# Performance work log

Hardware: AMD Instinct MI355X
Metric: run time of the kernel (lower is better)

## Reference

```python
import jax, jax.numpy as jnp
import numpy as np

NUM_HEADS = 8
NVIEW = 5
EPS = 1e-6


def setup_inputs() -> dict:
    key = jax.random.key(0)
    k1, k2, k3 = jax.random.split(key, 3)
    BV, HW, C = 20, 4096, 256
    x = jax.random.normal(k1, (BV, HW, C), dtype=jnp.float32)
    # torch.nn.Linear default init ~ U(-1/sqrt(in), 1/sqrt(in)); scale randn similarly
    W_qkv = jax.random.normal(k2, (C, 3 * C), dtype=jnp.float32) * (1.0 / np.sqrt(C))
    W_proj = jax.random.normal(k3, (C, C), dtype=jnp.float32) * (1.0 / np.sqrt(C))
    b_proj = jnp.zeros((C,), dtype=jnp.float32)
    return {"x": x, "W_qkv": W_qkv, "W_proj": W_proj, "b_proj": b_proj}


def reference(x, W_qkv, W_proj, b_proj):
    BV, HW, C = x.shape
    V = NVIEW
    B = BV // V
    H = NUM_HEADS
    d = C // H
    L = V * HW

    # merge views into one long sequence per batch element
    xb = x.reshape(B, L, C)

    # qkv projection (qkv_bias=False) -> [B, L, 3, H, d]
    qkv = (xb @ W_qkv).reshape(B, L, 3, H, d)
    q = qkv[:, :, 0]  # [B, L, H, d]
    k = qkv[:, :, 1]
    v = qkv[:, :, 2]

    # elu + 1 feature map, computed in float32 (as in the autocast-disabled block)
    q = (jax.nn.elu(q) + 1.0).astype(jnp.float32)
    k = (jax.nn.elu(k) + 1.0).astype(jnp.float32)
    v = v.astype(jnp.float32)

    # linear attention: kv = sum_l k_l (x) v_l  -> [B, H, m, d]
    kv = jnp.einsum('nlhd,nlhm->nhmd', k, v)
    # normalizer z = 1 / (q . sum_l k_l)  -> [B, L, H]
    k_sum = k.sum(axis=1)  # [B, H, d]
    z = 1.0 / (jnp.einsum('nlhd,nhd->nlh', q, k_sum) + EPS)
    # output y -> [B, L, H, m]
    y = jnp.einsum('nlhd,nhmd,nlh->nlhm', q, kv, z)

    y = y.reshape(BV, HW, C)
    return y @ W_proj + b_proj
```

## Files before the change

kernel.cpp:

```cpp
#include <hip/hip_runtime.h>

#define M_ROWS 81920
#define KDIM 256
#define NQKV 768
#define LROWS 20480
#define EPSV 1e-6f
#define KV_CHUNKS 160

using bf16x8 = __attribute__((ext_vector_type(8))) short;
using f32x4  = __attribute__((ext_vector_type(4))) float;

static __device__ __forceinline__ unsigned short f2bf(float f) {
  union { float f; unsigned int u; } c; c.f = f;
  unsigned int u = c.u;
  u += 0x7fff + ((u >> 16) & 1);
  return (unsigned short)(u >> 16);
}
static __device__ __forceinline__ float bf2f(unsigned short h) {
  union { unsigned int u; float f; } c; c.u = ((unsigned int)h) << 16;
  return c.f;
}

static __device__ __forceinline__ void async_cp16(const void* g, void* l) {
  __builtin_amdgcn_global_load_lds(
      (const __attribute__((address_space(1))) void*)(unsigned long long)g,
      (__attribute__((address_space(3))) void*)(unsigned int)(unsigned long long)l,
      16, 0, 0);
}

__global__ void cvt_x(const float* __restrict__ x, unsigned short* __restrict__ xb) {
  long i = ((long)blockIdx.x * blockDim.x + threadIdx.x) * 4;
  float4 v = *(const float4*)(x + i);
  ushort4 o;
  o.x = f2bf(v.x); o.y = f2bf(v.y); o.z = f2bf(v.z); o.w = f2bf(v.w);
  *(ushort4*)(xb + i) = o;
}

__global__ void transpose_w(const float* __restrict__ w, unsigned short* __restrict__ wt,
                            int K, int N) {
  int k = blockIdx.x;
  for (int n = threadIdx.x; n < N; n += blockDim.x)
    wt[(size_t)n * K + k] = f2bf(w[(size_t)k * N + n]);
}

template <int EPI>
__global__ __launch_bounds__(256, 3)
void gemm_bt(const unsigned short* __restrict__ A,
             const unsigned short* __restrict__ Bt,
             void* __restrict__ C,
             const float* __restrict__ bias,
             int N) {
  __shared__ unsigned short As[128 * 32];
  __shared__ unsigned short Bs[128 * 32];
  const int K = 256;
  int t = threadIdx.x;
  int lane = t & 63;
  int w = t >> 6;
  int m0 = blockIdx.y * 128;
  int n0 = blockIdx.x * 128;
  const unsigned short* Bp = Bt;
  if (EPI == 1) Bp += (size_t)(blockIdx.y / 160) * 256 * 256;

  f32x4 acc[4][4];
#pragma unroll
  for (int i = 0; i < 4; i++)
#pragma unroll
    for (int j = 0; j < 4; j++) acc[i][j] = (f32x4){0.f, 0.f, 0.f, 0.f};

  int wm = w & 1, wn = w >> 1;
  int fm = lane & 15;
  int fk = (lane >> 4) * 8;
  int r0a = t >> 2, p0 = t & 3;
  int r1a = (t + 256) >> 2, p1 = t & 3;

  for (int kt = 0; kt < 8; kt++) {
    int k0 = kt * 32;
    __syncthreads();
    async_cp16(A + (size_t)(m0 + r0a) * K + k0 + p0 * 8, As + (size_t)t * 8);
    async_cp16(A + (size_t)(m0 + r1a) * K + k0 + p1 * 8, As + (size_t)(t + 256) * 8);
    async_cp16(Bp + (size_t)(n0 + r0a) * K + k0 + p0 * 8, Bs + (size_t)t * 8);
    async_cp16(Bp + (size_t)(n0 + r1a) * K + k0 + p1 * 8, Bs + (size_t)(t + 256) * 8);
    __syncthreads();
    bf16x8 af[4], bfr[4];
#pragma unroll
    for (int i = 0; i < 4; i++)
      af[i] = *(const bf16x8*)(As + (wm * 64 + i * 16 + fm) * 32 + fk);
#pragma unroll
    for (int j = 0; j < 4; j++)
      bfr[j] = *(const bf16x8*)(Bs + (wn * 64 + j * 16 + fm) * 32 + fk);
#pragma unroll
    for (int i = 0; i < 4; i++)
#pragma unroll
      for (int j = 0; j < 4; j++)
        acc[i][j] = __builtin_amdgcn_mfma_f32_16x16x32_bf16(af[i], bfr[j], acc[i][j], 0, 0, 0);
  }

  int quad = lane >> 4;
  int col = lane & 15;
#pragma unroll
  for (int i = 0; i < 4; i++) {
#pragma unroll
    for (int j = 0; j < 4; j++) {
      int gm_base = m0 + wm * 64 + i * 16 + quad * 4;
      int gn = n0 + wn * 64 + j * 16 + col;
#pragma unroll
      for (int r = 0; r < 4; r++) {
        float v = acc[i][j][r];
        int gm = gm_base + r;
        if (EPI == 0) {
          if (gn < 512) v = (v > 0.f) ? v + 1.f : __expf(v);
          ((unsigned short*)C)[(size_t)gm * N + gn] = f2bf(v);
        } else {
          ((float*)C)[(size_t)gm * N + gn] = v + bias[gn];
        }
      }
    }
  }
}

__global__ __launch_bounds__(512)
void kv_reduce(const unsigned short* __restrict__ qkv, float* __restrict__ kvp) {
  __shared__ unsigned short s[32 * 512];
  int chunk = blockIdx.x;
  int n = blockIdx.y;
  int t = threadIdx.x;
  int lane = t & 63;
  int w = t >> 6;
  long r0 = (long)n * LROWS + (long)chunk * 128;

  float acc[4][4] = {};
  float ks[4] = {};
  int mg = lane >> 3;
  int m0 = mg * 4, d0 = (lane & 7) * 4;

  for (int tile = 0; tile < 4; tile++) {
    __syncthreads();
#pragma unroll
    for (int q = 0; q < 4; q++) {
      int c = t + q * 512;
      int row = c >> 6, part = c & 63;
      async_cp16(qkv + (size_t)(r0 + tile * 32 + row) * 768 + 256 + part * 8,
                 s + (size_t)c * 8);
    }
    __syncthreads();
#pragma unroll 4
    for (int row = 0; row < 32; row++) {
      ushort4 kk = *(const ushort4*)(s + row * 512 + w * 32 + d0);
      ushort4 vv = *(const ushort4*)(s + row * 512 + 256 + w * 32 + m0);
      float kf[4] = {bf2f(kk.x), bf2f(kk.y), bf2f(kk.z), bf2f(kk.w)};
      float vf[4] = {bf2f(vv.x), bf2f(vv.y), bf2f(vv.z), bf2f(vv.w)};
#pragma unroll
      for (int i = 0; i < 4; i++)
#pragma unroll
        for (int j = 0; j < 4; j++) acc[i][j] += vf[i] * kf[j];
      if (mg == 0) {
        ks[0] += kf[0]; ks[1] += kf[1]; ks[2] += kf[2]; ks[3] += kf[3];
      }
    }
  }
  float* o = kvp + ((size_t)(n * KV_CHUNKS + chunk) * 8 + w) * 1056;
#pragma unroll
  for (int i = 0; i < 4; i++)
#pragma unroll
    for (int j = 0; j < 4; j++) o[(m0 + i) * 32 + d0 + j] = acc[i][j];
  if (mg == 0) {
#pragma unroll
    for (int j = 0; j < 4; j++) o[1024 + d0 + j] = ks[j];
  }
}

__global__ __launch_bounds__(256)
void kv_combine(const float* __restrict__ kvp, float* __restrict__ kv,
                float* __restrict__ ksum) {
  int pair = blockIdx.x;
  int n = pair >> 3, h = pair & 7;
  int t = threadIdx.x;
  float a0 = 0.f, a1 = 0.f, a2 = 0.f, a3 = 0.f, a4 = 0.f;
  const float* base = kvp + ((size_t)(n * KV_CHUNKS) * 8 + h) * 1056;
  for (int c = 0; c < KV_CHUNKS; c++) {
    const float* p = base + (size_t)c * 8 * 1056;
    a0 += p[t]; a1 += p[t + 256]; a2 += p[t + 512]; a3 += p[t + 768];
    if (t < 32) a4 += p[1024 + t];
  }
  float* kvo = kv + (size_t)pair * 1024;
  kvo[t] = a0; kvo[t + 256] = a1; kvo[t + 512] = a2; kvo[t + 768] = a3;
  if (t < 32) ksum[pair * 32 + t] = a4;
}

__global__ __launch_bounds__(256)
void make_g(const float* __restrict__ kv, const float* __restrict__ wproj,
            unsigned short* __restrict__ gt) {
  __shared__ float kvs[1024];
  int pair = blockIdx.x;
  int n = pair >> 3, h = pair & 7;
  int c = threadIdx.x;
  for (int i = c; i < 1024; i += 256) kvs[i] = kv[(size_t)pair * 1024 + i];
  __syncthreads();
  float acc[32];
#pragma unroll
  for (int d = 0; d < 32; d++) acc[d] = 0.f;
  for (int m = 0; m < 32; m++) {
    float wp = wproj[(size_t)(h * 32 + m) * 256 + c];
#pragma unroll
    for (int d = 0; d < 32; d++) acc[d] += kvs[m * 32 + d] * wp;
  }
  unsigned short* o = gt + ((size_t)n * 256 + c) * 256 + h * 32;
#pragma unroll
  for (int d = 0; d < 32; d++) o[d] = f2bf(acc[d]);
}

__global__ __launch_bounds__(256)
void scale_q(const unsigned short* __restrict__ qkv, const float* __restrict__ ksum,
             unsigned short* __restrict__ qp) {
  int t = threadIdx.x;
  int lane32 = t & 31;
  int rsub = t >> 5;
  long r0 = (long)blockIdx.x * 64;
  for (int p = 0; p < 8; p++) {
    long r = r0 + p * 8 + rsub;
    int n = (int)(r / LROWS);
    const unsigned short* q = qkv + r * 768 + lane32 * 8;
    ushort4 a = *(const ushort4*)(q);
    ushort4 b = *(const ushort4*)(q + 4);
    float qf[8] = {bf2f(a.x), bf2f(a.y), bf2f(a.z), bf2f(a.w),
                   bf2f(b.x), bf2f(b.y), bf2f(b.z), bf2f(b.w)};
    const float* ks = ksum + n * 256 + lane32 * 8;
    float sacc = 0.f;
#pragma unroll
    for (int i = 0; i < 8; i++) sacc += qf[i] * ks[i];
    sacc += __shfl_xor(sacc, 1);
    sacc += __shfl_xor(sacc, 2);
    float z = 1.f / (sacc + EPSV);
    ushort4 oa, ob;
    oa.x = f2bf(qf[0] * z); oa.y = f2bf(qf[1] * z);
    oa.z = f2bf(qf[2] * z); oa.w = f2bf(qf[3] * z);
    ob.x = f2bf(qf[4] * z); ob.y = f2bf(qf[5] * z);
    ob.z = f2bf(qf[6] * z); ob.w = f2bf(qf[7] * z);
    unsigned short* o = qp + r * 256 + lane32 * 8;
    *(ushort4*)o = oa;
    *(ushort4*)(o + 4) = ob;
  }
}

extern "C" void kernel_launch(void* const* d_in, const int* in_sizes, int n_in,
                              void* d_out, int out_size, void* d_ws, size_t ws_size,
                              hipStream_t stream) {
  (void)in_sizes; (void)n_in; (void)out_size; (void)ws_size;
  const float* x = (const float*)d_in[0];
  const float* Wqkv = (const float*)d_in[1];
  const float* Wproj = (const float*)d_in[2];
  const float* bproj = (const float*)d_in[3];
  float* out = (float*)d_out;

  char* ws = (char*)d_ws;
  unsigned short* xbf    = (unsigned short*)(ws);
  float*          kvp    = (float*)(ws);
  unsigned short* wqkvt  = (unsigned short*)(ws + 41943040);
  unsigned short* qkv_bf = (unsigned short*)(ws + 42336256);
  float*          kv     = (float*)(ws + 168165376);
  float*          ksum   = (float*)(ws + 168296448);
  unsigned short* gt     = (unsigned short*)(ws + 168300544);
  unsigned short* qp     = (unsigned short*)(ws + 168824832);

  cvt_x<<<M_ROWS * KDIM / 1024, 256, 0, stream>>>(x, xbf);
  transpose_w<<<256, 256, 0, stream>>>(Wqkv, wqkvt, 256, 768);
  gemm_bt<0><<<dim3(NQKV / 128, M_ROWS / 128), 256, 0, stream>>>(xbf, wqkvt, qkv_bf, nullptr, NQKV);
  kv_reduce<<<dim3(KV_CHUNKS, 4), 512, 0, stream>>>(qkv_bf, kvp);
  kv_combine<<<32, 256, 0, stream>>>(kvp, kv, ksum);
  make_g<<<32, 256, 0, stream>>>(kv, Wproj, gt);
  scale_q<<<M_ROWS / 64, 256, 0, stream>>>(qkv_bf, ksum, qp);
  gemm_bt<1><<<dim3(2, M_ROWS / 128), 256, 0, stream>>>(qp, gt, out, bproj, 256);
}
```

Measured before the change: 350.3 us.

## Tile weight transpose, remap GEMM tiles per XCD, fragment-order LDS, split kv reduction

The weight transpose is rewritten to stage through shared memory so reads and writes are coalesced. Both GEMMs switch to a 1D grid whose block IDs map contiguous M tiles to each XCD for L2 locality. The LDS staging layout changes so each MFMA fragment is read as a contiguous 16-byte chunk per lane, which is meant to avoid bank conflicts. The 160-chunk kv combine is split into two stages so the first stage runs on 256 blocks instead of 32. This adds an extra kernel launch and an intermediate buffer in the workspace.

```diff
diff --git a/kernel.cpp b/kernel.cpp
--- a/kernel.cpp
+++ b/kernel.cpp
@@ -36,11 +36,26 @@
   *(ushort4*)(xb + i) = o;
 }
 
-__global__ void transpose_w(const float* __restrict__ w, unsigned short* __restrict__ wt,
-                            int K, int N) {
-  int k = blockIdx.x;
-  for (int n = threadIdx.x; n < N; n += blockDim.x)
-    wt[(size_t)n * K + k] = f2bf(w[(size_t)k * N + n]);
+__global__ __launch_bounds__(256)
+void transpose_w(const float* __restrict__ w, unsigned short* __restrict__ wt) {
+  __shared__ unsigned short lds[64][258];
+  int n0 = blockIdx.x * 64;
+  int t = threadIdx.x;
+#pragma unroll 4
+  for (int it = 0; it < 64; it++) {
+    int k = (t >> 6) + 4 * it;
+    int n = t & 63;
+    lds[n][k] = f2bf(w[(size_t)k * NQKV + n0 + n]);
+  }
+  __syncthreads();
+#pragma unroll
+  for (int it = 0; it < 16; it++) {
+    int idx = it * 256 + t;
+    int n = idx >> 6, c4 = (idx & 63) * 4;
+    ushort4 v;
+    v.x = lds[n][c4]; v.y = lds[n][c4 + 1]; v.z = lds[n][c4 + 2]; v.w = lds[n][c4 + 3];
+    *(ushort4*)(wt + (size_t)(n0 + n) * 256 + c4) = v;
+  }
 }
 
 template <int EPI>
@@ -48,18 +63,26 @@
 void gemm_bt(const unsigned short* __restrict__ A,
              const unsigned short* __restrict__ Bt,
              void* __restrict__ C,
-             const float* __restrict__ bias,
-             int N) {
+             const float* __restrict__ bias) {
   __shared__ unsigned short As[128 * 32];
   __shared__ unsigned short Bs[128 * 32];
   const int K = 256;
+  const int N = (EPI == 0) ? NQKV : 256;
+  const int NT = (EPI == 0) ? 6 : 2;
   int t = threadIdx.x;
   int lane = t & 63;
   int w = t >> 6;
-  int m0 = blockIdx.y * 128;
-  int n0 = blockIdx.x * 128;
+
+  int id = blockIdx.x;
+  int xcd = id & 7;
+  int local = id >> 3;
+  int mt = local / NT;
+  int nt = local - mt * NT;
+  int mtile = xcd * 80 + mt;
+  int m0 = mtile * 128;
+  int n0 = nt * 128;
   const unsigned short* Bp = Bt;
-  if (EPI == 1) Bp += (size_t)(blockIdx.y / 160) * 256 * 256;
+  if (EPI == 1) Bp += (size_t)(mtile / 160) * 256 * 256;
 
   f32x4 acc[4][4];
 #pragma unroll
@@ -68,26 +91,27 @@
     for (int j = 0; j < 4; j++) acc[i][j] = (f32x4){0.f, 0.f, 0.f, 0.f};
 
   int wm = w & 1, wn = w >> 1;
-  int fm = lane & 15;
-  int fk = (lane >> 4) * 8;
-  int r0a = t >> 2, p0 = t & 3;
-  int r1a = (t + 256) >> 2, p1 = t & 3;
+  int fm_s = lane & 15;
+  int p_s = lane >> 4;
 
   for (int kt = 0; kt < 8; kt++) {
     int k0 = kt * 32;
     __syncthreads();
-    async_cp16(A + (size_t)(m0 + r0a) * K + k0 + p0 * 8, As + (size_t)t * 8);
-    async_cp16(A + (size_t)(m0 + r1a) * K + k0 + p1 * 8, As + (size_t)(t + 256) * 8);
-    async_cp16(Bp + (size_t)(n0 + r0a) * K + k0 + p0 * 8, Bs + (size_t)t * 8);
-    async_cp16(Bp + (size_t)(n0 + r1a) * K + k0 + p1 * 8, Bs + (size_t)(t + 256) * 8);
+#pragma unroll
+    for (int q = 0; q < 2; q++) {
+      int g = w * 2 + q;
+      int row = g * 16 + fm_s;
+      async_cp16(A + (size_t)(m0 + row) * K + k0 + p_s * 8, As + (size_t)(g * 64 + lane) * 8);
+      async_cp16(Bp + (size_t)(n0 + row) * K + k0 + p_s * 8, Bs + (size_t)(g * 64 + lane) * 8);
+    }
     __syncthreads();
     bf16x8 af[4], bfr[4];
 #pragma unroll
     for (int i = 0; i < 4; i++)
-      af[i] = *(const bf16x8*)(As + (wm * 64 + i * 16 + fm) * 32 + fk);
+      af[i] = *(const bf16x8*)(As + (size_t)((i + 4 * wm) * 64 + lane) * 8);
 #pragma unroll
     for (int j = 0; j < 4; j++)
-      bfr[j] = *(const bf16x8*)(Bs + (wn * 64 + j * 16 + fm) * 32 + fk);
+      bfr[j] = *(const bf16x8*)(Bs + (size_t)((j + 4 * wn) * 64 + lane) * 8);
 #pragma unroll
     for (int i = 0; i < 4; i++)
 #pragma unroll
@@ -170,15 +194,33 @@
 }
 
 __global__ __launch_bounds__(256)
-void kv_combine(const float* __restrict__ kvp, float* __restrict__ kv,
-                float* __restrict__ ksum) {
-  int pair = blockIdx.x;
+void kv_combine1(const float* __restrict__ kvp, float* __restrict__ kvp2) {
+  int b = blockIdx.x;
+  int pair = b >> 3, o = b & 7;
   int n = pair >> 3, h = pair & 7;
   int t = threadIdx.x;
   float a0 = 0.f, a1 = 0.f, a2 = 0.f, a3 = 0.f, a4 = 0.f;
   const float* base = kvp + ((size_t)(n * KV_CHUNKS) * 8 + h) * 1056;
-  for (int c = 0; c < KV_CHUNKS; c++) {
-    const float* p = base + (size_t)c * 8 * 1056;
+  for (int j = 0; j < KV_CHUNKS / 8; j++) {
+    const float* p = base + (size_t)(o + 8 * j) * 8 * 1056;
+    a0 += p[t]; a1 += p[t + 256]; a2 += p[t + 512]; a3 += p[t + 768];
+    if (t < 32) a4 += p[1024 + t];
+  }
+  float* oo = kvp2 + (size_t)b * 1056;
+  oo[t] = a0; oo[t + 256] = a1; oo[t + 512] = a2; oo[t + 768] = a3;
+  if (t < 32) oo[1024 + t] = a4;
+}
+
+__global__ __launch_bounds__(256)
+void kv_combine2(const float* __restrict__ kvp2, float* __restrict__ kv,
+                 float* __restrict__ ksum) {
+  int pair = blockIdx.x;
+  int t = threadIdx.x;
+  float a0 = 0.f, a1 = 0.f, a2 = 0.f, a3 = 0.f, a4 = 0.f;
+  const float* base = kvp2 + (size_t)pair * 8 * 1056;
+#pragma unroll
+  for (int s = 0; s < 8; s++) {
+    const float* p = base + (size_t)s * 1056;
     a0 += p[t]; a1 += p[t + 256]; a2 += p[t + 512]; a3 += p[t + 768];
     if (t < 32) a4 += p[1024 + t];
   }
@@ -255,6 +297,7 @@
   char* ws = (char*)d_ws;
   unsigned short* xbf    = (unsigned short*)(ws);
   float*          kvp    = (float*)(ws);
+  float*          kvp2   = (float*)(ws + 33554432);
   unsigned short* wqkvt  = (unsigned short*)(ws + 41943040);
   unsigned short* qkv_bf = (unsigned short*)(ws + 42336256);
   float*          kv     = (float*)(ws + 168165376);
@@ -263,11 +306,12 @@
   unsigned short* qp     = (unsigned short*)(ws + 168824832);
 
   cvt_x<<<M_ROWS * KDIM / 1024, 256, 0, stream>>>(x, xbf);
-  transpose_w<<<256, 256, 0, stream>>>(Wqkv, wqkvt, 256, 768);
-  gemm_bt<0><<<dim3(NQKV / 128, M_ROWS / 128), 256, 0, stream>>>(xbf, wqkvt, qkv_bf, nullptr, NQKV);
+  transpose_w<<<NQKV / 64, 256, 0, stream>>>(Wqkv, wqkvt);
+  gemm_bt<0><<<3840, 256, 0, stream>>>(xbf, wqkvt, qkv_bf, nullptr);
   kv_reduce<<<dim3(KV_CHUNKS, 4), 512, 0, stream>>>(qkv_bf, kvp);
-  kv_combine<<<32, 256, 0, stream>>>(kvp, kv, ksum);
+  kv_combine1<<<256, 256, 0, stream>>>(kvp, kvp2);
+  kv_combine2<<<32, 256, 0, stream>>>(kvp2, kv, ksum);
   make_g<<<32, 256, 0, stream>>>(kv, Wproj, gt);
   scale_q<<<M_ROWS / 64, 256, 0, stream>>>(qkv_bf, ksum, qp);
-  gemm_bt<1><<<dim3(2, M_ROWS / 128), 256, 0, stream>>>(qp, gt, out, bproj, 256);
-}
+  gemm_bt<1><<<1280, 256, 0, stream>>>(qp, gt, out, bproj);
+}
```

Result: faster. 332.0 us (-5.2%).
